# Performance work log

Measured on AMD Instinct MI355X. Metric: run time of the kernel, lower is better.

The kernel has to match this reference:

```python
import jax, jax.numpy as jnp
import numpy as np

EMB_DIM = 1024
HEAD_SIZE = 64
SEQ = 2048
BATCH = 8


def setup_inputs() -> dict:
    key = jax.random.key(0)
    kx, kq, kk, kv = jax.random.split(key, 4)
    x = jax.random.normal(kx, (BATCH, SEQ, EMB_DIM), dtype=jnp.float32)
    # nn.Linear(E, H, bias=False): y = x @ W.T with W of shape [H, E]; store as [E, H]
    s = 1.0 / np.sqrt(EMB_DIM)
    Wq = jax.random.uniform(kq, (EMB_DIM, HEAD_SIZE), jnp.float32, -s, s)
    Wk = jax.random.uniform(kk, (EMB_DIM, HEAD_SIZE), jnp.float32, -s, s)
    Wv = jax.random.uniform(kv, (EMB_DIM, HEAD_SIZE), jnp.float32, -s, s)
    return {"x": x, "Wq": Wq, "Wk": Wk, "Wv": Wv}


def reference(x, Wq, Wk, Wv):
    B, S, E = x.shape
    q = jnp.einsum("bse,eh->bsh", x, Wq)
    k = jnp.einsum("bse,eh->bsh", x, Wk)
    v = jnp.einsum("bse,eh->bsh", x, Wv)
    # NOTE: original scales by E**-0.5 (embedding dim), not head_size**-0.5
    att = jnp.einsum("bqh,bkh->bqk", q, k) * (E ** -0.5)
    causal = jnp.tril(jnp.ones((S, S), dtype=bool))
    att = jnp.where(causal, att, -jnp.inf)
    att = jax.nn.softmax(att, axis=-1)
    # dropout(p=0.2) treated as identity (eval mode) for deterministic reference
    out = jnp.einsum("bqk,bkh->bqh", att, v)
    return out
```

## Files before the change

### kernel.cpp

```cpp
#include <hip/hip_runtime.h>

constexpr int Bn = 8, S = 2048, E = 1024, H = 64;
constexpr float SCALE = 0.03125f * 1.44269504f;

typedef __attribute__((ext_vector_type(8))) short short8;
typedef __attribute__((ext_vector_type(4))) float f32x4;

__device__ __forceinline__ unsigned short f2bf(float f) {
  unsigned u = __builtin_bit_cast(unsigned, f);
  u += 0x7fffu + ((u >> 16) & 1u);
  return (unsigned short)(u >> 16);
}
__device__ __forceinline__ ushort4 f4bf(float4 f) {
  return make_ushort4(f2bf(f.x), f2bf(f.y), f2bf(f.z), f2bf(f.w));
}

__global__ __launch_bounds__(256) void wtrans_kernel(
    const float* __restrict__ Wq, const float* __restrict__ Wk,
    const float* __restrict__ Wv, unsigned short* __restrict__ WT3) {
  __shared__ unsigned short tb[64][72];
  const int m = blockIdx.x >> 4;
  const int e0 = (blockIdx.x & 15) * 64;
  const float* W = (m == 0) ? Wq : (m == 1) ? Wk : Wv;
  const int t = threadIdx.x;
#pragma unroll
  for (int it = 0; it < 4; ++it) {
    int idx = t + it * 256;
    int r = idx >> 4, c4 = idx & 15;
    float4 f = ((const float4*)(W + (long)(e0 + r) * H))[c4];
    *(ushort4*)&tb[r][c4 * 4] = f4bf(f);
  }
  __syncthreads();
#pragma unroll
  for (int it = 0; it < 4; ++it) {
    int idx = t + it * 256;
    int h = idx >> 4, e4 = idx & 15;
    ushort4 u = make_ushort4(tb[e4 * 4 + 0][h], tb[e4 * 4 + 1][h],
                             tb[e4 * 4 + 2][h], tb[e4 * 4 + 3][h]);
    ((ushort4*)(WT3 + (long)(m * 64 + h) * E + e0))[e4] = u;
  }
}

__global__ __launch_bounds__(256) void qkv_kernel(
    const float* __restrict__ x, const unsigned short* __restrict__ WT3,
    unsigned short* __restrict__ q, unsigned short* __restrict__ kk,
    unsigned short* __restrict__ vT) {
  __shared__ unsigned short xs[32][136];
  __shared__ unsigned short ws[192][136];
  const int t = threadIdx.x;
  const int w = t >> 6, lane = t & 63, l15 = lane & 15, g = lane >> 4;
  const long row0 = (long)blockIdx.x * 32;
  const int xrow = t >> 5, xslot = t & 31;
  const int wrow = t >> 4, wslot = t & 15;

  f32x4 acc[2][3];
#pragma unroll
  for (int rt = 0; rt < 2; ++rt)
#pragma unroll
    for (int ct = 0; ct < 3; ++ct) acc[rt][ct] = f32x4{0.f, 0.f, 0.f, 0.f};

  float4 px[4];
  short8 pw[12];
#pragma unroll
  for (int it = 0; it < 4; ++it)
    px[it] = ((const float4*)(x + (row0 + xrow + it * 8) * E))[xslot];
#pragma unroll
  for (int it = 0; it < 12; ++it)
    pw[it] = *(const short8*)(WT3 + (long)(wrow + it * 16) * E + wslot * 8);
#pragma unroll
  for (int it = 0; it < 4; ++it)
    *(ushort4*)&xs[xrow + it * 8][xslot * 4] = f4bf(px[it]);
#pragma unroll
  for (int it = 0; it < 12; ++it)
    *(short8*)&ws[wrow + it * 16][wslot * 8] = pw[it];

  for (int c = 0; c < 8; ++c) {
    __syncthreads();
    if (c < 7) {
      const int e0 = (c + 1) * 128;
#pragma unroll
      for (int it = 0; it < 4; ++it)
        px[it] = ((const float4*)(x + (row0 + xrow + it * 8) * E + e0))[xslot];
#pragma unroll
      for (int it = 0; it < 12; ++it)
        pw[it] = *(const short8*)(WT3 + (long)(wrow + it * 16) * E + e0 + wslot * 8);
    }
#pragma unroll
    for (int kh = 0; kh < 4; ++kh) {
      short8 a0 = *(const short8*)&xs[l15][kh * 32 + g * 8];
      short8 a1 = *(const short8*)&xs[16 + l15][kh * 32 + g * 8];
#pragma unroll
      for (int ct = 0; ct < 3; ++ct) {
        short8 b = *(const short8*)&ws[w * 48 + ct * 16 + l15][kh * 32 + g * 8];
        acc[0][ct] = __builtin_amdgcn_mfma_f32_16x16x32_bf16(a0, b, acc[0][ct], 0, 0, 0);
        acc[1][ct] = __builtin_amdgcn_mfma_f32_16x16x32_bf16(a1, b, acc[1][ct], 0, 0, 0);
      }
    }
    __syncthreads();
    if (c < 7) {
#pragma unroll
      for (int it = 0; it < 4; ++it)
        *(ushort4*)&xs[xrow + it * 8][xslot * 4] = f4bf(px[it]);
#pragma unroll
      for (int it = 0; it < 12; ++it)
        *(short8*)&ws[wrow + it * 16][wslot * 8] = pw[it];
    }
  }

  const int bb = (int)(row0 >> 11);
  const int srow = (int)(row0 & 2047);
#pragma unroll
  for (int ct = 0; ct < 3; ++ct) {
    const int col = w * 48 + ct * 16 + l15;
    const int mm = col >> 6, ch = col & 63;
#pragma unroll
    for (int rt = 0; rt < 2; ++rt) {
      const int srl = rt * 16 + g * 4;
      if (mm == 0) {
#pragma unroll
        for (int r = 0; r < 4; ++r)
          q[(row0 + srl + r) * H + ch] = f2bf(acc[rt][ct][r] * SCALE);
      } else if (mm == 1) {
#pragma unroll
        for (int r = 0; r < 4; ++r)
          kk[(row0 + srl + r) * H + ch] = f2bf(acc[rt][ct][r]);
      } else {
        ushort4 v4 = make_ushort4(f2bf(acc[rt][ct][0]), f2bf(acc[rt][ct][1]),
                                  f2bf(acc[rt][ct][2]), f2bf(acc[rt][ct][3]));
        *(ushort4*)(vT + ((long)bb * H + ch) * S + srow + srl) = v4;
      }
    }
  }
}

__global__ __launch_bounds__(256, 3) void attn_kernel(
    const unsigned short* __restrict__ q, const unsigned short* __restrict__ k,
    const unsigned short* __restrict__ vT, float* __restrict__ out) {
  __shared__ unsigned short pl[4][16][72];
  __shared__ float Om[4][64][17];
  __shared__ float ms[4][16], ls[4][16];
  const int t = threadIdx.x;
  const int w = t >> 6, lane = t & 63, l15 = lane & 15, g = lane >> 4;
  const int b = blockIdx.x & 7, p = blockIdx.x >> 3;
  const int qt = 127 - p;
  const int qrow0 = qt * 16;
  const int nt = (qt >> 2) + 1;
  const unsigned short* kb = k + (long)b * S * H;
  const unsigned short* vb = vT + (long)b * H * S;

  const unsigned short* qp = q + ((long)b * S + qrow0 + l15) * H + g * 8;
  short8 bq0 = *(const short8*)qp;
  short8 bq1 = *(const short8*)(qp + 32);

  f32x4 O[4];
#pragma unroll
  for (int c = 0; c < 4; ++c) O[c] = f32x4{0.f, 0.f, 0.f, 0.f};
  float m_ = -1e30f, l_ = 0.f;

  short8 ak[4][2];
  int kt = w;
  if (kt < nt) {
#pragma unroll
    for (int c = 0; c < 4; ++c)
#pragma unroll
      for (int kh = 0; kh < 2; ++kh)
        ak[c][kh] = *(const short8*)(kb + (long)(kt * 64 + c * 16 + l15) * H + kh * 32 + g * 8);
  }

  for (; kt < nt; kt += 4) {
    short8 av[4][2];
#pragma unroll
    for (int c = 0; c < 4; ++c)
#pragma unroll
      for (int kh = 0; kh < 2; ++kh)
        av[c][kh] = *(const short8*)(vb + (long)(c * 16 + l15) * S + kt * 64 + kh * 32 + g * 8);
    f32x4 sc[4];
#pragma unroll
    for (int c = 0; c < 4; ++c) {
      sc[c] = f32x4{0.f, 0.f, 0.f, 0.f};
      sc[c] = __builtin_amdgcn_mfma_f32_16x16x32_bf16(ak[c][0], bq0, sc[c], 0, 0, 0);
      sc[c] = __builtin_amdgcn_mfma_f32_16x16x32_bf16(ak[c][1], bq1, sc[c], 0, 0, 0);
    }
    if (kt + 4 < nt) {
#pragma unroll
      for (int c = 0; c < 4; ++c)
#pragma unroll
        for (int kh = 0; kh < 2; ++kh)
          ak[c][kh] = *(const short8*)(kb + (long)((kt + 4) * 64 + c * 16 + l15) * H + kh * 32 + g * 8);
    }
    if (kt == nt - 1) {
#pragma unroll
      for (int c = 0; c < 4; ++c)
#pragma unroll
        for (int r = 0; r < 4; ++r)
          if (kt * 64 + c * 16 + g * 4 + r > qrow0 + l15) sc[c][r] = -1e30f;
    }
    float x0 = fmaxf(fmaxf(sc[0][0], sc[0][1]), fmaxf(sc[0][2], sc[0][3]));
    float x1 = fmaxf(fmaxf(sc[1][0], sc[1][1]), fmaxf(sc[1][2], sc[1][3]));
    float x2 = fmaxf(fmaxf(sc[2][0], sc[2][1]), fmaxf(sc[2][2], sc[2][3]));
    float x3 = fmaxf(fmaxf(sc[3][0], sc[3][1]), fmaxf(sc[3][2], sc[3][3]));
    float pmax = fmaxf(fmaxf(x0, x1), fmaxf(x2, x3));
    if (!__all(pmax - m_ <= 10.0f)) {
      float mx = fmaxf(pmax, __shfl_xor(pmax, 16));
      mx = fmaxf(mx, __shfl_xor(mx, 32));
      float mn = fmaxf(m_, mx);
      float al = exp2f(m_ - mn);
      l_ *= al;
#pragma unroll
      for (int c = 0; c < 4; ++c)
#pragma unroll
        for (int r = 0; r < 4; ++r) O[c][r] *= al;
      m_ = mn;
    }
#pragma unroll
    for (int c = 0; c < 4; ++c)
#pragma unroll
      for (int r = 0; r < 4; ++r) sc[c][r] = exp2f(sc[c][r] - m_);
    float s0 = (sc[0][0] + sc[0][1]) + (sc[0][2] + sc[0][3]);
    float s1 = (sc[1][0] + sc[1][1]) + (sc[1][2] + sc[1][3]);
    float s2 = (sc[2][0] + sc[2][1]) + (sc[2][2] + sc[2][3]);
    float s3 = (sc[3][0] + sc[3][1]) + (sc[3][2] + sc[3][3]);
    l_ += (s0 + s1) + (s2 + s3);
#pragma unroll
    for (int c = 0; c < 4; ++c) {
      ushort4 p4 = make_ushort4(f2bf(sc[c][0]), f2bf(sc[c][1]),
                                f2bf(sc[c][2]), f2bf(sc[c][3]));
      *(ushort4*)&pl[w][l15][c * 16 + g * 4] = p4;
    }
    short8 bp0 = *(const short8*)&pl[w][l15][g * 8];
    short8 bp1 = *(const short8*)&pl[w][l15][32 + g * 8];
#pragma unroll
    for (int c = 0; c < 4; ++c) {
      O[c] = __builtin_amdgcn_mfma_f32_16x16x32_bf16(av[c][0], bp0, O[c], 0, 0, 0);
      O[c] = __builtin_amdgcn_mfma_f32_16x16x32_bf16(av[c][1], bp1, O[c], 0, 0, 0);
    }
  }

  l_ += __shfl_xor(l_, 16);
  l_ += __shfl_xor(l_, 32);

  if (g == 0) { ms[w][l15] = m_; ls[w][l15] = l_; }
#pragma unroll
  for (int c = 0; c < 4; ++c)
#pragma unroll
    for (int r = 0; r < 4; ++r)
      Om[w][c * 16 + g * 4 + r][l15] = O[c][r];
  __syncthreads();
  {
    const int row = t >> 4, h0 = (t & 15) * 4;
    float m0 = ms[0][row], m1 = ms[1][row], m2 = ms[2][row], m3 = ms[3][row];
    float mstar = fmaxf(fmaxf(m0, m1), fmaxf(m2, m3));
    float f0 = exp2f(m0 - mstar), f1 = exp2f(m1 - mstar);
    float f2 = exp2f(m2 - mstar), f3 = exp2f(m3 - mstar);
    float inv = 1.0f / (ls[0][row] * f0 + ls[1][row] * f1 +
                        ls[2][row] * f2 + ls[3][row] * f3);
    float4 o;
    o.x = (Om[0][h0 + 0][row] * f0 + Om[1][h0 + 0][row] * f1 +
           Om[2][h0 + 0][row] * f2 + Om[3][h0 + 0][row] * f3) * inv;
    o.y = (Om[0][h0 + 1][row] * f0 + Om[1][h0 + 1][row] * f1 +
           Om[2][h0 + 1][row] * f2 + Om[3][h0 + 1][row] * f3) * inv;
    o.z = (Om[0][h0 + 2][row] * f0 + Om[1][h0 + 2][row] * f1 +
           Om[2][h0 + 2][row] * f2 + Om[3][h0 + 2][row] * f3) * inv;
    o.w = (Om[0][h0 + 3][row] * f0 + Om[1][h0 + 3][row] * f1 +
           Om[2][h0 + 3][row] * f2 + Om[3][h0 + 3][row] * f3) * inv;
    *(float4*)(out + ((long)b * S + qrow0 + row) * H + h0) = o;
  }
}

extern "C" void kernel_launch(void* const* d_in, const int* in_sizes, int n_in,
                              void* d_out, int out_size, void* d_ws, size_t ws_size,
                              hipStream_t stream) {
  const float* x  = (const float*)d_in[0];
  const float* Wq = (const float*)d_in[1];
  const float* Wk = (const float*)d_in[2];
  const float* Wv = (const float*)d_in[3];
  float* outp = (float*)d_out;
  unsigned short* WT3 = (unsigned short*)d_ws;
  unsigned short* q  = (unsigned short*)((char*)d_ws + 512 * 1024);
  unsigned short* kk = q + (size_t)Bn * S * H;
  unsigned short* vT = kk + (size_t)Bn * S * H;
  wtrans_kernel<<<dim3(48), dim3(256), 0, stream>>>(Wq, Wk, Wv, WT3);
  qkv_kernel<<<dim3((Bn * S) / 32), dim3(256), 0, stream>>>(x, WT3, q, kk, vT);
  attn_kernel<<<dim3(Bn * 128), dim3(256), 0, stream>>>(q, kk, vT, outp);
}
```

Before: 145.9 us.

## Widen attention key tile to 128 per wave and drop K prefetch

```diff
diff --git a/kernel.cpp b/kernel.cpp
--- a/kernel.cpp
+++ b/kernel.cpp
@@ -133,10 +133,10 @@
   }
 }
 
-__global__ __launch_bounds__(256, 3) void attn_kernel(
+__global__ __launch_bounds__(256, 2) void attn_kernel(
     const unsigned short* __restrict__ q, const unsigned short* __restrict__ k,
     const unsigned short* __restrict__ vT, float* __restrict__ out) {
-  __shared__ unsigned short pl[4][16][72];
+  __shared__ unsigned short pl[4][16][136];
   __shared__ float Om[4][64][17];
   __shared__ float ms[4][16], ls[4][16];
   const int t = threadIdx.x;
@@ -144,7 +144,7 @@
   const int b = blockIdx.x & 7, p = blockIdx.x >> 3;
   const int qt = 127 - p;
   const int qrow0 = qt * 16;
-  const int nt = (qt >> 2) + 1;
+  const int ntk = (qt + 8) >> 3;
   const unsigned short* kb = k + (long)b * S * H;
   const unsigned short* vb = vT + (long)b * H * S;
 
@@ -157,49 +157,44 @@
   for (int c = 0; c < 4; ++c) O[c] = f32x4{0.f, 0.f, 0.f, 0.f};
   float m_ = -1e30f, l_ = 0.f;
 
-  short8 ak[4][2];
-  int kt = w;
-  if (kt < nt) {
+  for (int kt = w; kt < ntk; kt += 4) {
+    const int k0 = kt * 128;
+    short8 ak[8][2];
+#pragma unroll
+    for (int c = 0; c < 8; ++c)
+#pragma unroll
+      for (int kh = 0; kh < 2; ++kh)
+        ak[c][kh] = *(const short8*)(kb + (long)(k0 + c * 16 + l15) * H + kh * 32 + g * 8);
+    short8 av[4][4];
 #pragma unroll
     for (int c = 0; c < 4; ++c)
 #pragma unroll
-      for (int kh = 0; kh < 2; ++kh)
-        ak[c][kh] = *(const short8*)(kb + (long)(kt * 64 + c * 16 + l15) * H + kh * 32 + g * 8);
-  }
-
-  for (; kt < nt; kt += 4) {
-    short8 av[4][2];
-#pragma unroll
-    for (int c = 0; c < 4; ++c)
-#pragma unroll
-      for (int kh = 0; kh < 2; ++kh)
-        av[c][kh] = *(const short8*)(vb + (long)(c * 16 + l15) * S + kt * 64 + kh * 32 + g * 8);
-    f32x4 sc[4];
-#pragma unroll
-    for (int c = 0; c < 4; ++c) {
+      for (int kh = 0; kh < 4; ++kh)
+        av[c][kh] = *(const short8*)(vb + (long)(c * 16 + l15) * S + k0 + kh * 32 + g * 8);
+    f32x4 sc[8];
+#pragma unroll
+    for (int c = 0; c < 8; ++c) {
       sc[c] = f32x4{0.f, 0.f, 0.f, 0.f};
       sc[c] = __builtin_amdgcn_mfma_f32_16x16x32_bf16(ak[c][0], bq0, sc[c], 0, 0, 0);
       sc[c] = __builtin_amdgcn_mfma_f32_16x16x32_bf16(ak[c][1], bq1, sc[c], 0, 0, 0);
     }
-    if (kt + 4 < nt) {
-#pragma unroll
-      for (int c = 0; c < 4; ++c)
-#pragma unroll
-        for (int kh = 0; kh < 2; ++kh)
-          ak[c][kh] = *(const short8*)(kb + (long)((kt + 4) * 64 + c * 16 + l15) * H + kh * 32 + g * 8);
-    }
-    if (kt == nt - 1) {
-#pragma unroll
-      for (int c = 0; c < 4; ++c)
+    if (kt == ntk - 1) {
+#pragma unroll
+      for (int c = 0; c < 8; ++c)
 #pragma unroll
         for (int r = 0; r < 4; ++r)
-          if (kt * 64 + c * 16 + g * 4 + r > qrow0 + l15) sc[c][r] = -1e30f;
+          if (k0 + c * 16 + g * 4 + r > qrow0 + l15) sc[c][r] = -1e30f;
     }
     float x0 = fmaxf(fmaxf(sc[0][0], sc[0][1]), fmaxf(sc[0][2], sc[0][3]));
     float x1 = fmaxf(fmaxf(sc[1][0], sc[1][1]), fmaxf(sc[1][2], sc[1][3]));
     float x2 = fmaxf(fmaxf(sc[2][0], sc[2][1]), fmaxf(sc[2][2], sc[2][3]));
     float x3 = fmaxf(fmaxf(sc[3][0], sc[3][1]), fmaxf(sc[3][2], sc[3][3]));
-    float pmax = fmaxf(fmaxf(x0, x1), fmaxf(x2, x3));
+    float x4 = fmaxf(fmaxf(sc[4][0], sc[4][1]), fmaxf(sc[4][2], sc[4][3]));
+    float x5 = fmaxf(fmaxf(sc[5][0], sc[5][1]), fmaxf(sc[5][2], sc[5][3]));
+    float x6 = fmaxf(fmaxf(sc[6][0], sc[6][1]), fmaxf(sc[6][2], sc[6][3]));
+    float x7 = fmaxf(fmaxf(sc[7][0], sc[7][1]), fmaxf(sc[7][2], sc[7][3]));
+    float pmax = fmaxf(fmaxf(fmaxf(x0, x1), fmaxf(x2, x3)),
+                       fmaxf(fmaxf(x4, x5), fmaxf(x6, x7)));
     if (!__all(pmax - m_ <= 10.0f)) {
       float mx = fmaxf(pmax, __shfl_xor(pmax, 16));
       mx = fmaxf(mx, __shfl_xor(mx, 32));
@@ -213,27 +208,33 @@
       m_ = mn;
     }
 #pragma unroll
-    for (int c = 0; c < 4; ++c)
+    for (int c = 0; c < 8; ++c)
 #pragma unroll
       for (int r = 0; r < 4; ++r) sc[c][r] = exp2f(sc[c][r] - m_);
     float s0 = (sc[0][0] + sc[0][1]) + (sc[0][2] + sc[0][3]);
     float s1 = (sc[1][0] + sc[1][1]) + (sc[1][2] + sc[1][3]);
     float s2 = (sc[2][0] + sc[2][1]) + (sc[2][2] + sc[2][3]);
     float s3 = (sc[3][0] + sc[3][1]) + (sc[3][2] + sc[3][3]);
-    l_ += (s0 + s1) + (s2 + s3);
-#pragma unroll
-    for (int c = 0; c < 4; ++c) {
+    float s4 = (sc[4][0] + sc[4][1]) + (sc[4][2] + sc[4][3]);
+    float s5 = (sc[5][0] + sc[5][1]) + (sc[5][2] + sc[5][3]);
+    float s6 = (sc[6][0] + sc[6][1]) + (sc[6][2] + sc[6][3]);
+    float s7 = (sc[7][0] + sc[7][1]) + (sc[7][2] + sc[7][3]);
+    l_ += ((s0 + s1) + (s2 + s3)) + ((s4 + s5) + (s6 + s7));
+#pragma unroll
+    for (int c = 0; c < 8; ++c) {
       ushort4 p4 = make_ushort4(f2bf(sc[c][0]), f2bf(sc[c][1]),
                                 f2bf(sc[c][2]), f2bf(sc[c][3]));
       *(ushort4*)&pl[w][l15][c * 16 + g * 4] = p4;
     }
-    short8 bp0 = *(const short8*)&pl[w][l15][g * 8];
-    short8 bp1 = *(const short8*)&pl[w][l15][32 + g * 8];
-#pragma unroll
-    for (int c = 0; c < 4; ++c) {
-      O[c] = __builtin_amdgcn_mfma_f32_16x16x32_bf16(av[c][0], bp0, O[c], 0, 0, 0);
-      O[c] = __builtin_amdgcn_mfma_f32_16x16x32_bf16(av[c][1], bp1, O[c], 0, 0, 0);
-    }
+    short8 bp[4];
+#pragma unroll
+    for (int kh = 0; kh < 4; ++kh)
+      bp[kh] = *(const short8*)&pl[w][l15][kh * 32 + g * 8];
+#pragma unroll
+    for (int c = 0; c < 4; ++c)
+#pragma unroll
+      for (int kh = 0; kh < 4; ++kh)
+        O[c] = __builtin_amdgcn_mfma_f32_16x16x32_bf16(av[c][kh], bp[kh], O[c], 0, 0, 0);
   }
 
   l_ += __shfl_xor(l_, 16);
```

New measurement: 149.9 us. 2.7% more time.

## Share double-buffered K/V tiles in LDS across eight query waves

Applied to the files above, without the earlier changes.

```diff
diff --git a/kernel.cpp b/kernel.cpp
--- a/kernel.cpp
+++ b/kernel.cpp
@@ -133,138 +133,135 @@
   }
 }
 
-__global__ __launch_bounds__(256, 3) void attn_kernel(
+__global__ __launch_bounds__(512) void attn_kernel(
     const unsigned short* __restrict__ q, const unsigned short* __restrict__ k,
     const unsigned short* __restrict__ vT, float* __restrict__ out) {
-  __shared__ unsigned short pl[4][16][72];
-  __shared__ float Om[4][64][17];
-  __shared__ float ms[4][16], ls[4][16];
+  __shared__ unsigned short Kl[2][64][64];
+  __shared__ unsigned short Vl[2][64][64];
+  __shared__ unsigned short pl[8][16][72];
   const int t = threadIdx.x;
   const int w = t >> 6, lane = t & 63, l15 = lane & 15, g = lane >> 4;
-  const int b = blockIdx.x & 7, p = blockIdx.x >> 3;
-  const int qt = 127 - p;
-  const int qrow0 = qt * 16;
-  const int nt = (qt >> 2) + 1;
+  const int b = blockIdx.x & 7, qb = blockIdx.x >> 3;
+  const int r0 = qb * 128;
+  const int ntile = 2 * qb + 2;
+  const int myNt = 2 * qb + (w >> 2) + 1;
+  const int qrow = r0 + w * 16 + l15;
   const unsigned short* kb = k + (long)b * S * H;
   const unsigned short* vb = vT + (long)b * H * S;
 
-  const unsigned short* qp = q + ((long)b * S + qrow0 + l15) * H + g * 8;
-  short8 bq0 = *(const short8*)qp;
-  short8 bq1 = *(const short8*)(qp + 32);
-
+  const int srow = t >> 3, scol = t & 7;
+  const int swz = (scol ^ (srow & 7)) * 8;
+
+  short8 bq0, bq1;
+  {
+    const unsigned short* qp = q + ((long)b * S + qrow) * H + g * 8;
+    bq0 = *(const short8*)qp;
+    bq1 = *(const short8*)(qp + 32);
+  }
   f32x4 O[4];
 #pragma unroll
   for (int c = 0; c < 4; ++c) O[c] = f32x4{0.f, 0.f, 0.f, 0.f};
   float m_ = -1e30f, l_ = 0.f;
 
-  short8 ak[4][2];
-  int kt = w;
-  if (kt < nt) {
-#pragma unroll
-    for (int c = 0; c < 4; ++c)
-#pragma unroll
-      for (int kh = 0; kh < 2; ++kh)
-        ak[c][kh] = *(const short8*)(kb + (long)(kt * 64 + c * 16 + l15) * H + kh * 32 + g * 8);
-  }
-
-  for (; kt < nt; kt += 4) {
-    short8 av[4][2];
-#pragma unroll
-    for (int c = 0; c < 4; ++c)
-#pragma unroll
-      for (int kh = 0; kh < 2; ++kh)
-        av[c][kh] = *(const short8*)(vb + (long)(c * 16 + l15) * S + kt * 64 + kh * 32 + g * 8);
-    f32x4 sc[4];
-#pragma unroll
-    for (int c = 0; c < 4; ++c) {
-      sc[c] = f32x4{0.f, 0.f, 0.f, 0.f};
-      sc[c] = __builtin_amdgcn_mfma_f32_16x16x32_bf16(ak[c][0], bq0, sc[c], 0, 0, 0);
-      sc[c] = __builtin_amdgcn_mfma_f32_16x16x32_bf16(ak[c][1], bq1, sc[c], 0, 0, 0);
-    }
-    if (kt + 4 < nt) {
+  const int rc0 = (g ^ (l15 & 7)) * 8;
+  const int rc1 = ((4 + g) ^ (l15 & 7)) * 8;
+
+  {
+    uint4 pk = *(const uint4*)(kb + ((long)srow << 6) + scol * 8);
+    uint4 pv = *(const uint4*)(vb + (long)srow * S + scol * 8);
+    *(uint4*)&Kl[0][srow][swz] = pk;
+    *(uint4*)&Vl[0][srow][swz] = pv;
+    __syncthreads();
+  }
+
+  for (int kt = 0; kt < ntile; ++kt) {
+    const int cur = kt & 1;
+    const int k0 = kt * 64;
+    const bool pf = (kt + 1 < ntile);
+    uint4 pk, pv;
+    if (pf) {
+      const int kn = k0 + 64;
+      pk = *(const uint4*)(kb + ((long)(kn + srow) << 6) + scol * 8);
+      pv = *(const uint4*)(vb + (long)srow * S + kn + scol * 8);
+    }
+    if (kt < myNt) {
+      short8 ak[4][2];
+#pragma unroll
+      for (int c = 0; c < 4; ++c) {
+        ak[c][0] = *(const short8*)&Kl[cur][c * 16 + l15][rc0];
+        ak[c][1] = *(const short8*)&Kl[cur][c * 16 + l15][rc1];
+      }
+      f32x4 sc[4];
+#pragma unroll
+      for (int c = 0; c < 4; ++c) {
+        sc[c] = f32x4{0.f, 0.f, 0.f, 0.f};
+        sc[c] = __builtin_amdgcn_mfma_f32_16x16x32_bf16(ak[c][0], bq0, sc[c], 0, 0, 0);
+        sc[c] = __builtin_amdgcn_mfma_f32_16x16x32_bf16(ak[c][1], bq1, sc[c], 0, 0, 0);
+      }
+      if (kt == myNt - 1) {
+#pragma unroll
+        for (int c = 0; c < 4; ++c)
+#pragma unroll
+          for (int r = 0; r < 4; ++r)
+            if (k0 + c * 16 + g * 4 + r > qrow) sc[c][r] = -1e30f;
+      }
+      float x0 = fmaxf(fmaxf(sc[0][0], sc[0][1]), fmaxf(sc[0][2], sc[0][3]));
+      float x1 = fmaxf(fmaxf(sc[1][0], sc[1][1]), fmaxf(sc[1][2], sc[1][3]));
+      float x2 = fmaxf(fmaxf(sc[2][0], sc[2][1]), fmaxf(sc[2][2], sc[2][3]));
+      float x3 = fmaxf(fmaxf(sc[3][0], sc[3][1]), fmaxf(sc[3][2], sc[3][3]));
+      float pmax = fmaxf(fmaxf(x0, x1), fmaxf(x2, x3));
+      if (!__all(pmax - m_ <= 10.0f)) {
+        float mx = fmaxf(pmax, __shfl_xor(pmax, 16));
+        mx = fmaxf(mx, __shfl_xor(mx, 32));
+        float mn = fmaxf(m_, mx);
+        float al = exp2f(m_ - mn);
+        l_ *= al;
+#pragma unroll
+        for (int c = 0; c < 4; ++c)
+#pragma unroll
+          for (int r = 0; r < 4; ++r) O[c][r] *= al;
+        m_ = mn;
+      }
 #pragma unroll
       for (int c = 0; c < 4; ++c)
 #pragma unroll
-        for (int kh = 0; kh < 2; ++kh)
-          ak[c][kh] = *(const short8*)(kb + (long)((kt + 4) * 64 + c * 16 + l15) * H + kh * 32 + g * 8);
-    }
-    if (kt == nt - 1) {
-#pragma unroll
-      for (int c = 0; c < 4; ++c)
-#pragma unroll
-        for (int r = 0; r < 4; ++r)
-          if (kt * 64 + c * 16 + g * 4 + r > qrow0 + l15) sc[c][r] = -1e30f;
-    }
-    float x0 = fmaxf(fmaxf(sc[0][0], sc[0][1]), fmaxf(sc[0][2], sc[0][3]));
-    float x1 = fmaxf(fmaxf(sc[1][0], sc[1][1]), fmaxf(sc[1][2], sc[1][3]));
-    float x2 = fmaxf(fmaxf(sc[2][0], sc[2][1]), fmaxf(sc[2][2], sc[2][3]));
-    float x3 = fmaxf(fmaxf(sc[3][0], sc[3][1]), fmaxf(sc[3][2], sc[3][3]));
-    float pmax = fmaxf(fmaxf(x0, x1), fmaxf(x2, x3));
-    if (!__all(pmax - m_ <= 10.0f)) {
-      float mx = fmaxf(pmax, __shfl_xor(pmax, 16));
-      mx = fmaxf(mx, __shfl_xor(mx, 32));
-      float mn = fmaxf(m_, mx);
-      float al = exp2f(m_ - mn);
-      l_ *= al;
-#pragma unroll
-      for (int c = 0; c < 4; ++c)
-#pragma unroll
-        for (int r = 0; r < 4; ++r) O[c][r] *= al;
-      m_ = mn;
-    }
-#pragma unroll
-    for (int c = 0; c < 4; ++c)
-#pragma unroll
-      for (int r = 0; r < 4; ++r) sc[c][r] = exp2f(sc[c][r] - m_);
-    float s0 = (sc[0][0] + sc[0][1]) + (sc[0][2] + sc[0][3]);
-    float s1 = (sc[1][0] + sc[1][1]) + (sc[1][2] + sc[1][3]);
-    float s2 = (sc[2][0] + sc[2][1]) + (sc[2][2] + sc[2][3]);
-    float s3 = (sc[3][0] + sc[3][1]) + (sc[3][2] + sc[3][3]);
-    l_ += (s0 + s1) + (s2 + s3);
-#pragma unroll
-    for (int c = 0; c < 4; ++c) {
-      ushort4 p4 = make_ushort4(f2bf(sc[c][0]), f2bf(sc[c][1]),
-                                f2bf(sc[c][2]), f2bf(sc[c][3]));
-      *(ushort4*)&pl[w][l15][c * 16 + g * 4] = p4;
-    }
-    short8 bp0 = *(const short8*)&pl[w][l15][g * 8];
-    short8 bp1 = *(const short8*)&pl[w][l15][32 + g * 8];
-#pragma unroll
-    for (int c = 0; c < 4; ++c) {
-      O[c] = __builtin_amdgcn_mfma_f32_16x16x32_bf16(av[c][0], bp0, O[c], 0, 0, 0);
-      O[c] = __builtin_amdgcn_mfma_f32_16x16x32_bf16(av[c][1], bp1, O[c], 0, 0, 0);
-    }
+        for (int r = 0; r < 4; ++r) sc[c][r] = exp2f(sc[c][r] - m_);
+      float s0 = (sc[0][0] + sc[0][1]) + (sc[0][2] + sc[0][3]);
+      float s1 = (sc[1][0] + sc[1][1]) + (sc[1][2] + sc[1][3]);
+      float s2 = (sc[2][0] + sc[2][1]) + (sc[2][2] + sc[2][3]);
+      float s3 = (sc[3][0] + sc[3][1]) + (sc[3][2] + sc[3][3]);
+      l_ += (s0 + s1) + (s2 + s3);
+#pragma unroll
+      for (int c = 0; c < 4; ++c) {
+        ushort4 p4 = make_ushort4(f2bf(sc[c][0]), f2bf(sc[c][1]),
+                                  f2bf(sc[c][2]), f2bf(sc[c][3]));
+        *(ushort4*)&pl[w][l15][c * 16 + g * 4] = p4;
+      }
+      short8 bp0 = *(const short8*)&pl[w][l15][g * 8];
+      short8 bp1 = *(const short8*)&pl[w][l15][32 + g * 8];
+#pragma unroll
+      for (int c = 0; c < 4; ++c) {
+        short8 av0 = *(const short8*)&Vl[cur][c * 16 + l15][rc0];
+        short8 av1 = *(const short8*)&Vl[cur][c * 16 + l15][rc1];
+        O[c] = __builtin_amdgcn_mfma_f32_16x16x32_bf16(av0, bp0, O[c], 0, 0, 0);
+        O[c] = __builtin_amdgcn_mfma_f32_16x16x32_bf16(av1, bp1, O[c], 0, 0, 0);
+      }
+    }
+    if (pf) {
+      *(uint4*)&Kl[cur ^ 1][srow][swz] = pk;
+      *(uint4*)&Vl[cur ^ 1][srow][swz] = pv;
+    }
+    __syncthreads();
   }
 
   l_ += __shfl_xor(l_, 16);
   l_ += __shfl_xor(l_, 32);
-
-  if (g == 0) { ms[w][l15] = m_; ls[w][l15] = l_; }
+  const float inv = 1.0f / l_;
+  float* op = out + ((long)b * S + qrow) * H + g * 4;
 #pragma unroll
   for (int c = 0; c < 4; ++c)
-#pragma unroll
-    for (int r = 0; r < 4; ++r)
-      Om[w][c * 16 + g * 4 + r][l15] = O[c][r];
-  __syncthreads();
-  {
-    const int row = t >> 4, h0 = (t & 15) * 4;
-    float m0 = ms[0][row], m1 = ms[1][row], m2 = ms[2][row], m3 = ms[3][row];
-    float mstar = fmaxf(fmaxf(m0, m1), fmaxf(m2, m3));
-    float f0 = exp2f(m0 - mstar), f1 = exp2f(m1 - mstar);
-    float f2 = exp2f(m2 - mstar), f3 = exp2f(m3 - mstar);
-    float inv = 1.0f / (ls[0][row] * f0 + ls[1][row] * f1 +
-                        ls[2][row] * f2 + ls[3][row] * f3);
-    float4 o;
-    o.x = (Om[0][h0 + 0][row] * f0 + Om[1][h0 + 0][row] * f1 +
-           Om[2][h0 + 0][row] * f2 + Om[3][h0 + 0][row] * f3) * inv;
-    o.y = (Om[0][h0 + 1][row] * f0 + Om[1][h0 + 1][row] * f1 +
-           Om[2][h0 + 1][row] * f2 + Om[3][h0 + 1][row] * f3) * inv;
-    o.z = (Om[0][h0 + 2][row] * f0 + Om[1][h0 + 2][row] * f1 +
-           Om[2][h0 + 2][row] * f2 + Om[3][h0 + 2][row] * f3) * inv;
-    o.w = (Om[0][h0 + 3][row] * f0 + Om[1][h0 + 3][row] * f1 +
-           Om[2][h0 + 3][row] * f2 + Om[3][h0 + 3][row] * f3) * inv;
-    *(float4*)(out + ((long)b * S + qrow0 + row) * H + h0) = o;
-  }
+    *(float4*)(op + c * 16) = make_float4(O[c][0] * inv, O[c][1] * inv,
+                                          O[c][2] * inv, O[c][3] * inv);
 }
 
 extern "C" void kernel_launch(void* const* d_in, const int* in_sizes, int n_in,
@@ -281,5 +278,5 @@
   unsigned short* vT = kk + (size_t)Bn * S * H;
   wtrans_kernel<<<dim3(48), dim3(256), 0, stream>>>(Wq, Wk, Wv, WT3);
   qkv_kernel<<<dim3((Bn * S) / 32), dim3(256), 0, stream>>>(x, WT3, q, kk, vT);
-  attn_kernel<<<dim3(Bn * 128), dim3(256), 0, stream>>>(q, kk, vT, outp);
-}
+  attn_kernel<<<dim3(Bn * 16), dim3(512), 0, stream>>>(q, kk, vT, outp);
+}
```

Measured after the change: 150.2 us. 1.03x slower.
